# Optimization experiments

Measured on AMD Instinct MI355X. Metric: run time of the kernel, lower is better.

Reference implementation:

```python
import jax, jax.numpy as jnp
import numpy as np

N_HEAD, D_K, D_V, D_MODEL = 16, 64, 64, 1024
LN_EPS = 1e-5


def setup_inputs() -> dict:
    key = jax.random.key(0)
    ks = jax.random.split(key, 13)
    B, S = 2, 2048
    s = 1.0 / np.sqrt(D_MODEL)
    return {
        "q": jax.random.normal(ks[0], (B, S, D_MODEL), jnp.float32),
        "k": jax.random.normal(ks[1], (B, S, D_MODEL), jnp.float32),
        "v": jax.random.normal(ks[2], (B, S, D_MODEL), jnp.float32),
        "Wq": jax.random.normal(ks[3], (D_MODEL, N_HEAD * D_K), jnp.float32) * s,
        "bq": jnp.zeros((N_HEAD * D_K,), jnp.float32),
        "Wk": jax.random.normal(ks[4], (D_MODEL, N_HEAD * D_K), jnp.float32) * s,
        "bk": jnp.zeros((N_HEAD * D_K,), jnp.float32),
        "Wv": jax.random.normal(ks[5], (D_MODEL, N_HEAD * D_V), jnp.float32) * s,
        "bv": jnp.zeros((N_HEAD * D_V,), jnp.float32),
        "Wo": jax.random.normal(ks[6], (N_HEAD * D_V, D_MODEL), jnp.float32) * s,
        "bo": jnp.zeros((D_MODEL,), jnp.float32),
        "ln_gamma": jnp.ones((D_MODEL,), jnp.float32),
        "ln_beta": jnp.zeros((D_MODEL,), jnp.float32),
    }


def reference(q, k, v, Wq, bq, Wk, bk, Wv, bv, Wo, bo, ln_gamma, ln_beta):
    B, S, _ = q.shape
    temperature = jnp.asarray(np.power(D_K, 0.5), q.dtype)
    # QKV projections -> [B, S, H, d]
    q_ = (q @ Wq + bq).reshape(B, S, N_HEAD, D_K)
    k_ = (k @ Wk + bk).reshape(B, S, N_HEAD, D_K)
    v_ = (v @ Wv + bv).reshape(B, S, N_HEAD, D_V)
    # scaled dot-product attention per head
    scores = jnp.einsum("bqhd,bkhd->bhqk", q_, k_) / temperature
    attn = jax.nn.softmax(scores, axis=-1)
    ctx = jnp.einsum("bhqk,bkhd->bqhd", attn, v_).reshape(B, S, N_HEAD * D_V)
    # output projection + residual + LayerNorm
    out = ctx @ Wo + bo + q
    mu = jnp.mean(out, axis=-1, keepdims=True)
    var = jnp.var(out, axis=-1, keepdims=True)
    out = (out - mu) * jax.lax.rsqrt(var + LN_EPS) * ln_gamma + ln_beta
    return out
```

## Files before the change

### kernel.cpp

```cpp
#include <hip/hip_runtime.h>
#include <hip/hip_bf16.h>

typedef float f32x4 __attribute__((ext_vector_type(4)));
typedef float f32x16 __attribute__((ext_vector_type(16)));
typedef __bf16 bf16x8 __attribute__((ext_vector_type(8)));
typedef __bf16 bf16x4 __attribute__((ext_vector_type(4)));
typedef unsigned u32x2 __attribute__((ext_vector_type(2)));

#define DM 1024
#define SL 2048
#define NHEAD 16
#define LOG2E 1.44269504088896f
#define EXP2(x) __builtin_amdgcn_exp2f(x)

static __device__ __forceinline__ f32x4 mfma16(bf16x8 a, bf16x8 b, f32x4 c) {
    return __builtin_amdgcn_mfma_f32_16x16x32_bf16(a, b, c, 0, 0, 0);
}
static __device__ __forceinline__ f32x16 mfma32(bf16x8 a, bf16x8 b, f32x16 c) {
    return __builtin_amdgcn_mfma_f32_32x32x16_bf16(a, b, c, 0, 0, 0);
}

static __device__ __forceinline__ void gload16(const void* g, void* l) {
    __builtin_amdgcn_global_load_lds(
        (const __attribute__((address_space(1))) unsigned*)g,
        (__attribute__((address_space(3))) unsigned*)l, 16, 0, 0);
}

static __device__ __forceinline__ unsigned packbf(float lo, float hi) {
    unsigned short lu = __builtin_bit_cast(unsigned short, (__bf16)lo);
    unsigned short hu = __builtin_bit_cast(unsigned short, (__bf16)hi);
    return ((unsigned)hu << 16) | (unsigned)lu;
}

__global__ __launch_bounds__(256) void cast_kernel(
    const float* __restrict__ x0, const float* __restrict__ x1, const float* __restrict__ x2,
    __bf16* __restrict__ y0, __bf16* __restrict__ y1, __bf16* __restrict__ y2)
{
    const float* x = (blockIdx.y == 0) ? x0 : (blockIdx.y == 1) ? x1 : x2;
    __bf16* y = (blockIdx.y == 0) ? y0 : (blockIdx.y == 1) ? y1 : y2;
    size_t i = ((size_t)blockIdx.x * 256 + threadIdx.x) * 8;
    float4 a = *reinterpret_cast<const float4*>(&x[i]);
    float4 b = *reinterpret_cast<const float4*>(&x[i + 4]);
    bf16x8 o;
    o[0] = (__bf16)a.x; o[1] = (__bf16)a.y; o[2] = (__bf16)a.z; o[3] = (__bf16)a.w;
    o[4] = (__bf16)b.x; o[5] = (__bf16)b.y; o[6] = (__bf16)b.z; o[7] = (__bf16)b.w;
    *reinterpret_cast<bf16x8*>(&y[i]) = o;
}

__global__ __launch_bounds__(256) void wt4_kernel(
    const float* __restrict__ W0, const float* __restrict__ W1,
    const float* __restrict__ W2, const float* __restrict__ W3,
    __bf16* __restrict__ T0, __bf16* __restrict__ T1,
    __bf16* __restrict__ T2, __bf16* __restrict__ T3)
{
    const float* W = (blockIdx.z == 0) ? W0 : (blockIdx.z == 1) ? W1
                   : (blockIdx.z == 2) ? W2 : W3;
    __bf16* Wt = (blockIdx.z == 0) ? T0 : (blockIdx.z == 1) ? T1
               : (blockIdx.z == 2) ? T2 : T3;
    __shared__ float tle[32][33];
    const int tx = threadIdx.x, ty = threadIdx.y;
    const int n0 = blockIdx.x * 32, k0 = blockIdx.y * 32;
#pragma unroll
    for (int i = 0; i < 4; ++i) {
        int r = ty + 8 * i;
        tle[r][tx] = W[(size_t)(k0 + r) * DM + (n0 + tx)];
    }
    __syncthreads();
#pragma unroll
    for (int i = 0; i < 4; ++i) {
        int r = ty + 8 * i;
        Wt[(size_t)(n0 + r) * DM + (k0 + tx)] = (__bf16)tle[tx][r];
    }
}

static __device__ __forceinline__ void gemm_body_bf16(
    const __bf16* __restrict__ A, const __bf16* __restrict__ Wt,
    const float* __restrict__ bias, const float* __restrict__ resid,
    __bf16* __restrict__ Yb, float* __restrict__ Yf,
    int mode, float oscale, int r0, int c0)
{
    __shared__ __attribute__((aligned(16))) __bf16 As[128 * 64];
    __shared__ __attribute__((aligned(16))) __bf16 Bs[128 * 64];
    const int t = threadIdx.x;
    const int w = t >> 6, lane = t & 63;
    const int l15 = lane & 15, lhi = lane >> 4;
    const int wr = w >> 1, wc = w & 1;
    const int lrow = lane >> 3;
    const int lcolswz = (((lane & 7) ^ lrow) << 3);
    const int jb = w * 4;
    const int swzr = (l15 & 7) << 3;

    const f32x4 fzero = {0.f, 0.f, 0.f, 0.f};
    f32x4 acc[4][4];
#pragma unroll
    for (int m = 0; m < 4; ++m)
#pragma unroll
        for (int n = 0; n < 4; ++n) acc[m][n] = fzero;

    const __bf16* gA = &A[(size_t)(r0 + jb * 8 + lrow) * DM + lcolswz];
    const __bf16* gB = &Wt[(size_t)(c0 + jb * 8 + lrow) * DM + lcolswz];

    for (int kt = 0; kt < DM; kt += 64) {
        __syncthreads();
#pragma unroll
        for (int i = 0; i < 4; ++i) {
            gload16(gA + (size_t)i * 8 * DM + kt, &As[(jb + i) * 512]);
            gload16(gB + (size_t)i * 8 * DM + kt, &Bs[(jb + i) * 512]);
        }
        __syncthreads();
#pragma unroll
        for (int kk = 0; kk < 2; ++kk) {
            bf16x8 af[4], bfr[4];
#pragma unroll
            for (int m = 0; m < 4; ++m)
                af[m] = *reinterpret_cast<const bf16x8*>(
                    &As[(wr * 64 + m * 16 + l15) * 64 + ((kk * 32 + lhi * 8) ^ swzr)]);
#pragma unroll
            for (int n = 0; n < 4; ++n)
                bfr[n] = *reinterpret_cast<const bf16x8*>(
                    &Bs[(wc * 64 + n * 16 + l15) * 64 + ((kk * 32 + lhi * 8) ^ swzr)]);
#pragma unroll
            for (int m = 0; m < 4; ++m)
#pragma unroll
                for (int n = 0; n < 4; ++n)
                    acc[m][n] = mfma16(af[m], bfr[n], acc[m][n]);
        }
    }
#pragma unroll
    for (int m = 0; m < 4; ++m)
#pragma unroll
        for (int n = 0; n < 4; ++n)
#pragma unroll
            for (int r = 0; r < 4; ++r) {
                int grow = r0 + wr * 64 + m * 16 + lhi * 4 + r;
                int gcol = c0 + wc * 64 + n * 16 + l15;
                float val = acc[m][n][r] + bias[gcol];
                if (mode == 0) {
                    Yb[(size_t)grow * DM + gcol] = (__bf16)(val * oscale);
                } else if (mode == 1) {
                    int bb = grow >> 11, ss = grow & (SL - 1);
                    int hh = gcol >> 6, dd = gcol & 63;
                    Yb[(((size_t)(bb * NHEAD + hh)) * 64 + dd) * SL + ss] = (__bf16)val;
                } else {
                    size_t idx = (size_t)grow * DM + gcol;
                    Yf[idx] = val + resid[idx];
                }
            }
}

__global__ __launch_bounds__(256) void qkv_kernel(
    const __bf16* __restrict__ xq, const __bf16* __restrict__ xk, const __bf16* __restrict__ xv,
    const __bf16* __restrict__ WtQ, const __bf16* __restrict__ WtK, const __bf16* __restrict__ WtV,
    const float* __restrict__ bq, const float* __restrict__ bk, const float* __restrict__ bv,
    __bf16* __restrict__ Qp, __bf16* __restrict__ Kp, __bf16* __restrict__ Vt)
{
    const int p = blockIdx.x;
    const int logical = (p & 7) * 96 + (p >> 3);
    const int x = logical & 7;
    const int s = logical >> 3;
    const int y = s & 31, z = s >> 5;
    const __bf16* X = (z == 0) ? xq : (z == 1) ? xk : xv;
    const __bf16* Wt = (z == 0) ? WtQ : (z == 1) ? WtK : WtV;
    const float* bias = (z == 0) ? bq : (z == 1) ? bk : bv;
    __bf16* Yb = (z == 0) ? Qp : (z == 1) ? Kp : Vt;
    int mode = (z == 2) ? 1 : 0;
    float oscale = (z == 0) ? (0.125f * LOG2E) : 1.0f;
    gemm_body_bf16(X, Wt, bias, nullptr, Yb, nullptr, mode, oscale,
                   y * 128, x * 128);
}

__global__ __launch_bounds__(256) void oproj_kernel(
    const __bf16* __restrict__ Cxb, const __bf16* __restrict__ WtO,
    const float* __restrict__ bo, const float* __restrict__ resid,
    float* __restrict__ pre)
{
    const int p = blockIdx.x;
    const int logical = (p & 7) * 32 + (p >> 3);
    const int x = logical & 7, y = logical >> 3;
    gemm_body_bf16(Cxb, WtO, bo, resid, nullptr, pre, 2, 1.0f,
                   y * 128, x * 128);
}

__global__ __launch_bounds__(512, 4) void attn_kernel(
    const __bf16* __restrict__ Qp, const __bf16* __restrict__ Kp,
    const __bf16* __restrict__ Vt, __bf16* __restrict__ Op, float2* __restrict__ ML)
{
    __shared__ __attribute__((aligned(16))) __bf16 Kl[2][4096];
    __shared__ __attribute__((aligned(16))) __bf16 Vl[2][4096];
    const int t = threadIdx.x;
    const int w = t >> 6, lane = t & 63;
    const int l31 = lane & 31, hi = lane >> 5;

    const int id = blockIdx.x;
    const int logical = (id & 7) * 64 + (id >> 3);
    const int bh = logical >> 4, rr = logical & 15;
    const int qs = rr >> 1, half = rr & 1;
    const int b = bh >> 4, h = bh & 15;
    const size_t tokQ = (size_t)b * SL + qs * 256 + w * 32;
    const size_t kbase = (size_t)b * SL + half * 1024;
    const size_t vrow0 = (size_t)bh * 64;

    const int srow = t >> 3, scol = (t & 7) << 3;
    const __bf16* gK = &Kp[(kbase + srow) * DM + h * 64 + scol];
    const __bf16* gV = &Vt[(vrow0 + srow) * SL + half * 1024 + scol];
    const int sidx = ((srow * 128 + scol * 2) ^ ((srow & 7) << 4)) >> 1;

    bf16x8 bq[4];
#pragma unroll
    for (int ks = 0; ks < 4; ++ks)
        bq[ks] = *reinterpret_cast<const bf16x8*>(
            &Qp[(tokQ + l31) * DM + h * 64 + ks * 16 + hi * 8]);

    f32x16 o0, o1;
#pragma unroll
    for (int r = 0; r < 16; ++r) { o0[r] = 0.f; o1[r] = 0.f; }
    float m_run = -1e30f, l_run = 0.f;

    const int swz = (l31 & 7) << 4;
    const int NT = 1024 / 64;

    {
        bf16x8 kv = *reinterpret_cast<const bf16x8*>(gK);
        bf16x8 vv = *reinterpret_cast<const bf16x8*>(gV);
        *reinterpret_cast<bf16x8*>(&Kl[0][sidx]) = kv;
        *reinterpret_cast<bf16x8*>(&Vl[0][sidx]) = vv;
    }

    for (int ti = 0; ti < NT; ++ti) {
        const int cb = ti & 1;
        const bool pf = (ti + 1 < NT);
        bf16x8 kvn, vvn;
        if (pf) {
            kvn = *reinterpret_cast<const bf16x8*>(gK + (size_t)(ti + 1) * 64 * DM);
            vvn = *reinterpret_cast<const bf16x8*>(gV + (ti + 1) * 64);
        }
        __syncthreads();

        f32x16 c0, c1;
#pragma unroll
        for (int r = 0; r < 16; ++r) { c0[r] = 0.f; c1[r] = 0.f; }
        __builtin_amdgcn_s_setprio(1);
#pragma unroll
        for (int ks = 0; ks < 4; ++ks) {
            int off = ks * 32 + hi * 16;
            bf16x8 ak0 = *reinterpret_cast<const bf16x8*>(&Kl[cb][((l31 * 128 + off) ^ swz) >> 1]);
            bf16x8 ak1 = *reinterpret_cast<const bf16x8*>(&Kl[cb][(((32 + l31) * 128 + off) ^ swz) >> 1]);
            c0 = mfma32(ak0, bq[ks], c0);
            c1 = mfma32(ak1, bq[ks], c1);
        }
        __builtin_amdgcn_s_setprio(0);

        float mx[8];
#pragma unroll
        for (int r = 0; r < 8; ++r)
            mx[r] = fmaxf(fmaxf(c0[r], c0[r + 8]), fmaxf(c1[r], c1[r + 8]));
#pragma unroll
        for (int r = 0; r < 4; ++r) mx[r] = fmaxf(mx[r], mx[r + 4]);
        float tm = fmaxf(fmaxf(mx[0], mx[1]), fmaxf(mx[2], mx[3]));
        tm = fmaxf(tm, __shfl_xor(tm, 32));

        if (__any(tm > m_run + 11.5f)) {
            float nm = fmaxf(m_run, tm);
            float sc = EXP2(m_run - nm);
            m_run = nm;
            l_run *= sc;
#pragma unroll
            for (int r = 0; r < 16; ++r) {
                float sq = __shfl(sc, (r & 3) + 8 * (r >> 2) + 4 * hi);
                o0[r] *= sq; o1[r] *= sq;
            }
        }

        float s4a = 0.f, s4b = 0.f, s4c = 0.f, s4d = 0.f;
#pragma unroll
        for (int r = 0; r < 16; r += 4) {
            c0[r]     = EXP2(c0[r]     - m_run); s4a += c0[r];
            c0[r + 1] = EXP2(c0[r + 1] - m_run); s4b += c0[r + 1];
            c0[r + 2] = EXP2(c0[r + 2] - m_run); s4c += c0[r + 2];
            c0[r + 3] = EXP2(c0[r + 3] - m_run); s4d += c0[r + 3];
        }
#pragma unroll
        for (int r = 0; r < 16; r += 4) {
            c1[r]     = EXP2(c1[r]     - m_run); s4a += c1[r];
            c1[r + 1] = EXP2(c1[r + 1] - m_run); s4b += c1[r + 1];
            c1[r + 2] = EXP2(c1[r + 2] - m_run); s4c += c1[r + 2];
            c1[r + 3] = EXP2(c1[r + 3] - m_run); s4d += c1[r + 3];
        }
        float rs = (s4a + s4b) + (s4c + s4d);
        rs += __shfl_xor(rs, 32);
        l_run += rs;

        unsigned wd0[8], wd1[8];
#pragma unroll
        for (int tt = 0; tt < 4; ++tt)
#pragma unroll
            for (int p = 0; p < 2; ++p) {
                wd0[tt * 2 + p] = packbf(c0[4 * tt + 2 * p], c0[4 * tt + 2 * p + 1]);
                wd1[tt * 2 + p] = packbf(c1[4 * tt + 2 * p], c1[4 * tt + 2 * p + 1]);
            }
        unsigned ua[4][4];
#pragma unroll
        for (int s = 0; s < 4; ++s) {
            int tA = (s & 1) * 2;
#pragma unroll
            for (int p = 0; p < 2; ++p) {
                unsigned va = (s < 2) ? wd0[tA * 2 + p] : wd1[tA * 2 + p];
                unsigned vb = (s < 2) ? wd0[(tA + 1) * 2 + p] : wd1[(tA + 1) * 2 + p];
                u32x2 rres = __builtin_amdgcn_permlane32_swap(va, vb, false, false);
                ua[s][p] = rres[0]; ua[s][2 + p] = rres[1];
            }
        }

        __builtin_amdgcn_s_setprio(1);
#pragma unroll
        for (int s = 0; s < 4; ++s) {
            bf16x8 as = *reinterpret_cast<const bf16x8*>(&ua[s][0]);
            bf16x8 vf0 = *reinterpret_cast<const bf16x8*>(
                &Vl[cb][((l31 * 128 + s * 32 + hi * 16) ^ swz) >> 1]);
            bf16x8 vf1 = *reinterpret_cast<const bf16x8*>(
                &Vl[cb][(((32 + l31) * 128 + s * 32 + hi * 16) ^ swz) >> 1]);
            o0 = mfma32(as, vf0, o0);
            o1 = mfma32(as, vf1, o1);
        }
        __builtin_amdgcn_s_setprio(0);

        if (pf) {
            *reinterpret_cast<bf16x8*>(&Kl[cb ^ 1][sidx]) = kvn;
            *reinterpret_cast<bf16x8*>(&Vl[cb ^ 1][sidx]) = vvn;
        }
    }

    if (hi == 0)
        ML[((size_t)half * 4096 + tokQ + l31) * NHEAD + h] = float2{m_run, l_run};
    const size_t obase = (size_t)half * 4096 * DM;
#pragma unroll
    for (int r = 0; r < 16; ++r) {
        int qq = (r & 3) + 8 * (r >> 2) + 4 * hi;
        size_t rowi = obase + (tokQ + qq) * DM + h * 64;
        Op[rowi + l31]      = (__bf16)o0[r];
        Op[rowi + 32 + l31] = (__bf16)o1[r];
    }
}

__global__ __launch_bounds__(256) void combine_kernel(
    const __bf16* __restrict__ Op, const float2* __restrict__ ML,
    __bf16* __restrict__ Cxb)
{
    const size_t e = ((size_t)blockIdx.x * 256 + threadIdx.x) * 8;
    const int token = (int)(e >> 10);
    const int h = (int)((e >> 6) & 15);
    float2 ml0 = ML[(size_t)token * NHEAD + h];
    float2 ml1 = ML[((size_t)4096 + token) * NHEAD + h];
    float M = fmaxf(ml0.x, ml1.x);
    float s0 = EXP2(ml0.x - M), s1 = EXP2(ml1.x - M);
    float inv = 1.f / (ml0.y * s0 + ml1.y * s1);
    s0 *= inv; s1 *= inv;
    bf16x8 a0 = *reinterpret_cast<const bf16x8*>(&Op[e]);
    bf16x8 a1 = *reinterpret_cast<const bf16x8*>(&Op[(size_t)4096 * DM + e]);
    bf16x8 o;
#pragma unroll
    for (int j = 0; j < 8; ++j)
        o[j] = (__bf16)((float)a0[j] * s0 + (float)a1[j] * s1);
    *reinterpret_cast<bf16x8*>(&Cxb[e]) = o;
}

__global__ __launch_bounds__(256) void ln_kernel(
    const float* __restrict__ X, const float* __restrict__ gamma,
    const float* __restrict__ beta, float* __restrict__ out)
{
    const int row = blockIdx.x, t = threadIdx.x;
    float4 v = *reinterpret_cast<const float4*>(&X[(size_t)row * DM + t * 4]);
    float s = v.x + v.y + v.z + v.w;
    float s2 = v.x * v.x + v.y * v.y + v.z * v.z + v.w * v.w;
#pragma unroll
    for (int off = 1; off < 64; off <<= 1) {
        s += __shfl_xor(s, off);
        s2 += __shfl_xor(s2, off);
    }
    __shared__ float rs[4], rs2[4];
    const int w = t >> 6;
    if ((t & 63) == 0) { rs[w] = s; rs2[w] = s2; }
    __syncthreads();
    s = rs[0] + rs[1] + rs[2] + rs[3];
    s2 = rs2[0] + rs2[1] + rs2[2] + rs2[3];
    float mean = s * (1.f / DM);
    float var = s2 * (1.f / DM) - mean * mean;
    float rstd = rsqrtf(var + 1e-5f);
    int c = t * 4;
    float4 o;
    o.x = (v.x - mean) * rstd * gamma[c + 0] + beta[c + 0];
    o.y = (v.y - mean) * rstd * gamma[c + 1] + beta[c + 1];
    o.z = (v.z - mean) * rstd * gamma[c + 2] + beta[c + 2];
    o.w = (v.w - mean) * rstd * gamma[c + 3] + beta[c + 3];
    *reinterpret_cast<float4*>(&out[(size_t)row * DM + c]) = o;
}

extern "C" void kernel_launch(void* const* d_in, const int* in_sizes, int n_in,
                              void* d_out, int out_size, void* d_ws, size_t ws_size,
                              hipStream_t stream) {
    (void)in_sizes; (void)n_in; (void)out_size; (void)ws_size;
    const float* q   = (const float*)d_in[0];
    const float* k   = (const float*)d_in[1];
    const float* v   = (const float*)d_in[2];
    const float* Wq  = (const float*)d_in[3];
    const float* bq  = (const float*)d_in[4];
    const float* Wk  = (const float*)d_in[5];
    const float* bk  = (const float*)d_in[6];
    const float* Wv  = (const float*)d_in[7];
    const float* bv  = (const float*)d_in[8];
    const float* Wo  = (const float*)d_in[9];
    const float* bo  = (const float*)d_in[10];
    const float* lng = (const float*)d_in[11];
    const float* lnb = (const float*)d_in[12];

    char* ws = (char*)d_ws;
    const size_t MB = (size_t)1 << 20;
    __bf16* WtQ = (__bf16*)(ws + 0 * MB);
    __bf16* WtK = (__bf16*)(ws + 2 * MB);
    __bf16* WtV = (__bf16*)(ws + 4 * MB);
    __bf16* WtO = (__bf16*)(ws + 6 * MB);
    __bf16* Xbq = (__bf16*)(ws + 8 * MB);
    __bf16* Xbk = (__bf16*)(ws + 16 * MB);
    __bf16* Xbv = (__bf16*)(ws + 24 * MB);
    __bf16* Qp  = (__bf16*)(ws + 32 * MB);
    __bf16* Kp  = (__bf16*)(ws + 40 * MB);
    __bf16* Vt  = (__bf16*)(ws + 48 * MB);
    __bf16* Cxb = (__bf16*)(ws + 56 * MB);
    __bf16* Op  = (__bf16*)(ws + 8 * MB);
    float2* ML  = (float2*)(ws + 24 * MB);
    float*  pre = (float*)(ws + 8 * MB);

    cast_kernel<<<dim3(2048, 3), 256, 0, stream>>>(q, k, v, Xbq, Xbk, Xbv);
    wt4_kernel<<<dim3(32, 32, 4), dim3(32, 8), 0, stream>>>(
        Wq, Wk, Wv, Wo, WtQ, WtK, WtV, WtO);

    qkv_kernel<<<dim3(768), 256, 0, stream>>>(Xbq, Xbk, Xbv, WtQ, WtK, WtV,
                                              bq, bk, bv, Qp, Kp, Vt);
    attn_kernel<<<dim3(512), 512, 0, stream>>>(Qp, Kp, Vt, Op, ML);
    combine_kernel<<<dim3(2048), 256, 0, stream>>>(Op, ML, Cxb);
    oproj_kernel<<<dim3(256), 256, 0, stream>>>(Cxb, WtO, bo, q, pre);
    ln_kernel<<<4096, 256, 0, stream>>>(pre, lng, lnb, (float*)d_out);
}
```

Before: 163.9 us.

## Vectorize V-transpose stores, use 128x64 O-proj tiles, move K/V LDS stores earlier

The QKV GEMM epilogue is split by mode. The transposed V output now writes four consecutive tokens as one packed bf16x4 store instead of four scalar strided stores. The output projection gets its own kernel with 128x64 tiles and 512 blocks, which fills more of the device's compute units than 256 blocks of 128x128. In attention, the prefetched K/V registers are written to the other LDS buffer before the PV MFMAs rather than after, which may hide LDS write latency but raises register pressure during the MFMA section.

```diff
diff --git a/kernel.cpp b/kernel.cpp
--- a/kernel.cpp
+++ b/kernel.cpp
@@ -75,8 +75,8 @@
 
 static __device__ __forceinline__ void gemm_body_bf16(
     const __bf16* __restrict__ A, const __bf16* __restrict__ Wt,
-    const float* __restrict__ bias, const float* __restrict__ resid,
-    __bf16* __restrict__ Yb, float* __restrict__ Yf,
+    const float* __restrict__ bias,
+    __bf16* __restrict__ Yb,
     int mode, float oscale, int r0, int c0)
 {
     __shared__ __attribute__((aligned(16))) __bf16 As[128 * 64];
@@ -126,26 +126,35 @@
                     acc[m][n] = mfma16(af[m], bfr[n], acc[m][n]);
         }
     }
-#pragma unroll
-    for (int m = 0; m < 4; ++m)
-#pragma unroll
-        for (int n = 0; n < 4; ++n)
-#pragma unroll
-            for (int r = 0; r < 4; ++r) {
-                int grow = r0 + wr * 64 + m * 16 + lhi * 4 + r;
+    if (mode == 0) {
+#pragma unroll
+        for (int m = 0; m < 4; ++m)
+#pragma unroll
+            for (int n = 0; n < 4; ++n)
+#pragma unroll
+                for (int r = 0; r < 4; ++r) {
+                    int grow = r0 + wr * 64 + m * 16 + lhi * 4 + r;
+                    int gcol = c0 + wc * 64 + n * 16 + l15;
+                    Yb[(size_t)grow * DM + gcol] =
+                        (__bf16)((acc[m][n][r] + bias[gcol]) * oscale);
+                }
+    } else {
+#pragma unroll
+        for (int m = 0; m < 4; ++m)
+#pragma unroll
+            for (int n = 0; n < 4; ++n) {
+                int token = r0 + wr * 64 + m * 16 + lhi * 4;
                 int gcol = c0 + wc * 64 + n * 16 + l15;
-                float val = acc[m][n][r] + bias[gcol];
-                if (mode == 0) {
-                    Yb[(size_t)grow * DM + gcol] = (__bf16)(val * oscale);
-                } else if (mode == 1) {
-                    int bb = grow >> 11, ss = grow & (SL - 1);
-                    int hh = gcol >> 6, dd = gcol & 63;
-                    Yb[(((size_t)(bb * NHEAD + hh)) * 64 + dd) * SL + ss] = (__bf16)val;
-                } else {
-                    size_t idx = (size_t)grow * DM + gcol;
-                    Yf[idx] = val + resid[idx];
-                }
+                int bb = token >> 11, ss = token & (SL - 1);
+                int hh = gcol >> 6, dd = gcol & 63;
+                float bv = bias[gcol];
+                bf16x4 pv;
+#pragma unroll
+                for (int r = 0; r < 4; ++r) pv[r] = (__bf16)(acc[m][n][r] + bv);
+                *reinterpret_cast<bf16x4*>(
+                    &Yb[(((size_t)(bb * NHEAD + hh)) * 64 + dd) * SL + ss]) = pv;
             }
+    }
 }
 
 __global__ __launch_bounds__(256) void qkv_kernel(
@@ -165,8 +174,7 @@
     __bf16* Yb = (z == 0) ? Qp : (z == 1) ? Kp : Vt;
     int mode = (z == 2) ? 1 : 0;
     float oscale = (z == 0) ? (0.125f * LOG2E) : 1.0f;
-    gemm_body_bf16(X, Wt, bias, nullptr, Yb, nullptr, mode, oscale,
-                   y * 128, x * 128);
+    gemm_body_bf16(X, Wt, bias, Yb, mode, oscale, y * 128, x * 128);
 }
 
 __global__ __launch_bounds__(256) void oproj_kernel(
@@ -174,11 +182,70 @@
     const float* __restrict__ bo, const float* __restrict__ resid,
     float* __restrict__ pre)
 {
+    __shared__ __attribute__((aligned(16))) __bf16 As[128 * 64];
+    __shared__ __attribute__((aligned(16))) __bf16 Bs[64 * 64];
     const int p = blockIdx.x;
-    const int logical = (p & 7) * 32 + (p >> 3);
-    const int x = logical & 7, y = logical >> 3;
-    gemm_body_bf16(Cxb, WtO, bo, resid, nullptr, pre, 2, 1.0f,
-                   y * 128, x * 128);
+    const int logical = (p & 7) * 64 + (p >> 3);
+    const int x = logical & 15, y = logical >> 4;
+    const int r0 = y * 128, c0 = x * 64;
+
+    const int t = threadIdx.x;
+    const int w = t >> 6, lane = t & 63;
+    const int l15 = lane & 15, lhi = lane >> 4;
+    const int wr = w >> 1, wc = w & 1;
+    const int lrow = lane >> 3;
+    const int lcolswz = (((lane & 7) ^ lrow) << 3);
+    const int jb = w * 4, jb2 = w * 2;
+    const int swzr = (l15 & 7) << 3;
+
+    const f32x4 fzero = {0.f, 0.f, 0.f, 0.f};
+    f32x4 acc[4][2];
+#pragma unroll
+    for (int m = 0; m < 4; ++m)
+#pragma unroll
+        for (int n = 0; n < 2; ++n) acc[m][n] = fzero;
+
+    const __bf16* gA = &Cxb[(size_t)(r0 + jb * 8 + lrow) * DM + lcolswz];
+    const __bf16* gB = &WtO[(size_t)(c0 + jb2 * 8 + lrow) * DM + lcolswz];
+
+    for (int kt = 0; kt < DM; kt += 64) {
+        __syncthreads();
+#pragma unroll
+        for (int i = 0; i < 4; ++i)
+            gload16(gA + (size_t)i * 8 * DM + kt, &As[(jb + i) * 512]);
+#pragma unroll
+        for (int i = 0; i < 2; ++i)
+            gload16(gB + (size_t)i * 8 * DM + kt, &Bs[(jb2 + i) * 512]);
+        __syncthreads();
+#pragma unroll
+        for (int kk = 0; kk < 2; ++kk) {
+            bf16x8 af[4], bfr[2];
+#pragma unroll
+            for (int m = 0; m < 4; ++m)
+                af[m] = *reinterpret_cast<const bf16x8*>(
+                    &As[(wr * 64 + m * 16 + l15) * 64 + ((kk * 32 + lhi * 8) ^ swzr)]);
+#pragma unroll
+            for (int n = 0; n < 2; ++n)
+                bfr[n] = *reinterpret_cast<const bf16x8*>(
+                    &Bs[(wc * 32 + n * 16 + l15) * 64 + ((kk * 32 + lhi * 8) ^ swzr)]);
+#pragma unroll
+            for (int m = 0; m < 4; ++m)
+#pragma unroll
+                for (int n = 0; n < 2; ++n)
+                    acc[m][n] = mfma16(af[m], bfr[n], acc[m][n]);
+        }
+    }
+#pragma unroll
+    for (int m = 0; m < 4; ++m)
+#pragma unroll
+        for (int n = 0; n < 2; ++n)
+#pragma unroll
+            for (int r = 0; r < 4; ++r) {
+                int grow = r0 + wr * 64 + m * 16 + lhi * 4 + r;
+                int gcol = c0 + wc * 32 + n * 16 + l15;
+                size_t idx = (size_t)grow * DM + gcol;
+                pre[idx] = acc[m][n][r] + bo[gcol] + resid[idx];
+            }
 }
 
 __global__ __launch_bounds__(512, 4) void attn_kernel(
@@ -290,6 +357,11 @@
         rs += __shfl_xor(rs, 32);
         l_run += rs;
 
+        if (pf) {
+            *reinterpret_cast<bf16x8*>(&Kl[cb ^ 1][sidx]) = kvn;
+            *reinterpret_cast<bf16x8*>(&Vl[cb ^ 1][sidx]) = vvn;
+        }
+
         unsigned wd0[8], wd1[8];
 #pragma unroll
         for (int tt = 0; tt < 4; ++tt)
@@ -323,11 +395,6 @@
             o1 = mfma32(as, vf1, o1);
         }
         __builtin_amdgcn_s_setprio(0);
-
-        if (pf) {
-            *reinterpret_cast<bf16x8*>(&Kl[cb ^ 1][sidx]) = kvn;
-            *reinterpret_cast<bf16x8*>(&Vl[cb ^ 1][sidx]) = vvn;
-        }
     }
 
     if (hi == 0)
@@ -438,6 +505,6 @@
                                               bq, bk, bv, Qp, Kp, Vt);
     attn_kernel<<<dim3(512), 512, 0, stream>>>(Qp, Kp, Vt, Op, ML);
     combine_kernel<<<dim3(2048), 256, 0, stream>>>(Op, ML, Cxb);
-    oproj_kernel<<<dim3(256), 256, 0, stream>>>(Cxb, WtO, bo, q, pre);
+    oproj_kernel<<<dim3(512), 256, 0, stream>>>(Cxb, WtO, bo, q, pre);
     ln_kernel<<<4096, 256, 0, stream>>>(pre, lng, lnb, (float*)d_out);
 }
```

New measurement: 147.6 us. 1.11x faster.
